# Kernel optimization log

Hardware: AMD Instinct MI355X
Metric: run time of the kernel (lower is better)

The kernel has to match this reference:

```python
import jax, jax.numpy as jnp
import numpy as np

B, V, T = 256, 4, 512
N = 128          # num_notes_per_voice[0]
H = 256          # lstm_hidden_size
HL = 200         # hidden_size_linear
L = 2            # num_layers


def _scalar_lstm_last(x, Wih, Whh, b):
    """Stacked LSTM(input=1, hidden=1, layers=L) over x:(M,T) -> last output (M,).
    Wih, Whh, b: (L, 4) scalar weights per gate (i,f,g,o order, PyTorch biases summed)."""
    M = x.shape[0]
    h0 = jnp.zeros((L, M), x.dtype)
    c0 = jnp.zeros((L, M), x.dtype)

    def step(carry, xt):
        h, c = carry
        inp = xt
        hs, cs = [], []
        for l in range(L):
            g = Wih[l][:, None] * inp[None, :] + Whh[l][:, None] * h[l][None, :] + b[l][:, None]  # (4, M)
            i, f, gg, o = jax.nn.sigmoid(g[0]), jax.nn.sigmoid(g[1]), jnp.tanh(g[2]), jax.nn.sigmoid(g[3])
            cn = f * c[l] + i * gg
            hn = o * jnp.tanh(cn)
            hs.append(hn); cs.append(cn)
            inp = hn
        return (jnp.stack(hs), jnp.stack(cs)), None

    (h, _), _ = jax.lax.scan(step, (h0, c0), x.T)  # scan over time
    return h[-1]  # top layer final hidden, (M,)


def _lstm2_last(x, Wih0, Whh0, b0, Wih1, Whh1, b1):
    """2-layer LSTM(input=1, hidden=H) over x:(B,S,1) -> last top-layer hidden (B,H)."""
    Bs = x.shape[0]
    Hd = Whh0.shape[1]

    def cell(pre, c):
        i, f, g, o = jnp.split(pre, 4, axis=-1)
        cn = jax.nn.sigmoid(f) * c + jax.nn.sigmoid(i) * jnp.tanh(g)
        return jax.nn.sigmoid(o) * jnp.tanh(cn), cn

    z = jnp.zeros((Bs, Hd), x.dtype)

    def step(carry, xt):
        h0, c0, h1, c1 = carry
        h0n, c0n = cell(xt @ Wih0.T + h0 @ Whh0.T + b0, c0)
        h1n, c1n = cell(h0n @ Wih1.T + h1 @ Whh1.T + b1, c1)
        return (h0n, c0n, h1n, c1n), None

    (_, _, h1, _), _ = jax.lax.scan(step, (z, z, z, z), x.transpose(1, 0, 2))
    return h1


def _branch(tokens, tW, tU, tb, Wih0, Whh0, b0, Wih1, Whh1, b1):
    """Fused version of the per-class Python loop: one-hot each of N classes over
    time (voice 0 only, as in the source), run scalar LSTM per (batch, class),
    then 2-layer LSTM over the class axis. tokens: (B, T) int."""
    Bs, Ts = tokens.shape
    onehot = (tokens[:, :, None] == jnp.arange(N)[None, None, :]).astype(jnp.float32)  # (B,T,N)
    x = onehot.transpose(0, 2, 1).reshape(Bs * N, Ts)           # (B*N, T): one series per class
    states = _scalar_lstm_last(x, tW, tU, tb).reshape(Bs, N, 1)  # States_ln / States_rn
    return _lstm2_last(states, Wih0, Whh0, b0, Wih1, Whh1, b1)   # (B, H)


def setup_inputs() -> dict:
    key = jax.random.key(0)
    ks = iter(jax.random.split(key, 32))
    def rn_(shape, s=0.1):
        return jax.random.normal(next(ks), shape, dtype=jnp.float32) * s
    inp = {
        "ln": jax.random.randint(next(ks), (B, V, T), 0, N),
        "cn": jax.random.randint(next(ks), (B, V - 1), 0, N),
        "rn": jax.random.randint(next(ks), (B, V, T), 0, N),
        "metas": jax.random.randint(next(ks), (B, 3, T), 0, 16),
        # time_lstm_left/right: LSTM(1->1), L layers; biases summed into one
        "tl_Wih": rn_((L, 4), 0.5), "tl_Whh": rn_((L, 4), 0.5), "tl_b": rn_((L, 4), 0.5),
        "tr_Wih": rn_((L, 4), 0.5), "tr_Whh": rn_((L, 4), 0.5), "tr_b": rn_((L, 4), 0.5),
        # notes_lstm_left/right: 2-layer LSTM(1->H)
        "nl_Wih0": rn_((4 * H, 1)), "nl_Whh0": rn_((4 * H, H)), "nl_b0": rn_((4 * H,)),
        "nl_Wih1": rn_((4 * H, H)), "nl_Whh1": rn_((4 * H, H)), "nl_b1": rn_((4 * H,)),
        "nr_Wih0": rn_((4 * H, 1)), "nr_Whh0": rn_((4 * H, H)), "nr_b0": rn_((4 * H,)),
        "nr_Wih1": rn_((4 * H, H)), "nr_Whh1": rn_((4 * H, H)), "nr_b1": rn_((4 * H,)),
        # mlp_predictions: Linear(2H -> HL) -> ReLU -> Linear(HL -> N)
        "mW1": rn_((HL, 2 * H)), "mb1": rn_((HL,)),
        "mW2": rn_((N, HL)), "mb2": rn_((N,)),
    }
    return inp


def reference(ln, cn, rn, metas,
              tl_Wih, tl_Whh, tl_b, tr_Wih, tr_Whh, tr_b,
              nl_Wih0, nl_Whh0, nl_b0, nl_Wih1, nl_Whh1, nl_b1,
              nr_Wih0, nr_Whh0, nr_b0, nr_Wih1, nr_Whh1, nr_b1,
              mW1, mb1, mW2, mb2):
    # cn and metas are unpacked but unused in the original forward()
    note_pred_ln = _branch(ln[:, 0, :], tl_Wih, tl_Whh, tl_b,
                           nl_Wih0, nl_Whh0, nl_b0, nl_Wih1, nl_Whh1, nl_b1)
    note_pred_rn = _branch(rn[:, 0, :], tr_Wih, tr_Whh, tr_b,
                           nr_Wih0, nr_Whh0, nr_b0, nr_Wih1, nr_Whh1, nr_b1)
    h = jnp.concatenate([note_pred_ln, note_pred_rn], axis=1)   # (B, 2H)
    return jax.nn.relu(h @ mW1.T + mb1) @ mW2.T + mb2           # (B, N)
```

## Files before the change

### kernel.cpp

```cpp
#include <hip/hip_runtime.h>


typedef _Float16 f16;
typedef __attribute__((ext_vector_type(4))) _Float16 f16x4;
typedef __attribute__((ext_vector_type(8))) _Float16 f16x8;
typedef __attribute__((ext_vector_type(4))) float f32x4;
typedef unsigned long long u64;

#define NBATCH 256
#define NTIME  512
#define NCLS   128
#define NHID   256

__device__ __forceinline__ float sigf(float x) {
    return __builtin_amdgcn_rcpf(1.0f + __expf(-x));
}
__device__ __forceinline__ float tanh_f(float x) {
    return fmaf(2.0f, __builtin_amdgcn_rcpf(1.0f + __expf(-2.0f * x)), -1.0f);
}
__device__ __forceinline__ f16x4 LO(f16x8 v) { f16x4 r; r[0]=v[0]; r[1]=v[1]; r[2]=v[2]; r[3]=v[3]; return r; }
__device__ __forceinline__ f16x4 HI(f16x8 v) { f16x4 r; r[0]=v[4]; r[1]=v[5]; r[2]=v[6]; r[3]=v[7]; return r; }

__device__ __forceinline__ u64 ld_llc(const u64* p) {
    return __hip_atomic_load(p, __ATOMIC_RELAXED, __HIP_MEMORY_SCOPE_AGENT);
}
__device__ __forceinline__ void st_llc(u64* p, u64 v) {
    __hip_atomic_store(p, v, __ATOMIC_RELAXED, __HIP_MEMORY_SCOPE_AGENT);
}
__device__ __forceinline__ int ld_flag(const int* p) {
    return __hip_atomic_load(p, __ATOMIC_RELAXED, __HIP_MEMORY_SCOPE_AGENT);
}
__device__ __forceinline__ void st_flag(int* p, int v) {
    __hip_atomic_store(p, v, __ATOMIC_RELAXED, __HIP_MEMORY_SCOPE_AGENT);
}

struct P6 {
    const float* s0; const float* s1; const float* s2;
    const float* s3; const float* s4; const float* s5;
};

__global__ __launch_bounds__(256) void k_cvt(P6 p, f16* __restrict__ dst) {
    int i = blockIdx.x * 256 + threadIdx.x;
    int seg = i >> 18, d = i & 262143;
    const float* s = seg == 0 ? p.s0 : seg == 1 ? p.s1 : seg == 2 ? p.s2
                   : seg == 3 ? p.s3 : seg == 4 ? p.s4 : p.s5;
    const int e  = d & 7;
    const int fr = (d >> 3) & 15;
    const int fq = (d >> 7) & 3;
    const int ktp = (d >> 9) & 7;
    const int fi = (d >> 12) & 15;
    const int g  = (d >> 16) & 3;
    const int row = g * 256 + fi * 16 + fr;
    const int col = ktp * 32 + (e >> 2) * 16 + fq * 4 + (e & 3);
    dst[i] = (f16)s[row * 256 + col];
}

__global__ void k_zero(int* __restrict__ f) { f[blockIdx.x * 1024 + threadIdx.x] = 0; }

__global__ __launch_bounds__(128) void k_scalar_lstm(
    const int* __restrict__ ln, const int* __restrict__ rn,
    const float* __restrict__ tlW, const float* __restrict__ tlU, const float* __restrict__ tlb,
    const float* __restrict__ trW, const float* __restrict__ trU, const float* __restrict__ trb,
    float* __restrict__ states)
{
    __shared__ int tok[NTIME];
    const int bid = blockIdx.x;
    const int branch = bid >> 8;
    const int b = bid & 255;
    const int* tp = (branch ? rn : ln) + (size_t)b * (4 * NTIME);
    for (int i = threadIdx.x; i < NTIME; i += 128) tok[i] = tp[i];
    __syncthreads();
    const float* W  = branch ? trW : tlW;
    const float* U  = branch ? trU : tlU;
    const float* Bb = branch ? trb : tlb;
    const float u00 = U[0], u01 = U[1], u02 = U[2], u03 = U[3];
    const float f00 = Bb[0], f01 = Bb[1], f02 = Bb[2], f03 = Bb[3];
    const float o00 = f00 + W[0], o01 = f01 + W[1], o02 = f02 + W[2], o03 = f03 + W[3];
    const float w10 = W[4], w11 = W[5], w12 = W[6], w13 = W[7];
    const float u10 = U[4], u11 = U[5], u12 = U[6], u13 = U[7];
    const float b10 = Bb[4], b11 = Bb[5], b12 = Bb[6], b13 = Bb[7];
    const int n = threadIdx.x;
    float h0 = 0.f, c0 = 0.f, h1 = 0.f, c1 = 0.f;
    for (int t = 0; t < NTIME; ++t) {
        const bool x = (tok[t] == n);
        float pi = fmaf(u00, h0, x ? o00 : f00);
        float pf = fmaf(u01, h0, x ? o01 : f01);
        float pg = fmaf(u02, h0, x ? o02 : f02);
        float po = fmaf(u03, h0, x ? o03 : f03);
        float ig = sigf(pi), fg = sigf(pf), gg = tanh_f(pg), og = sigf(po);
        c0 = fmaf(fg, c0, ig * gg);
        h0 = og * tanh_f(c0);
        pi = fmaf(w10, h0, fmaf(u10, h1, b10));
        pf = fmaf(w11, h0, fmaf(u11, h1, b11));
        pg = fmaf(w12, h0, fmaf(u12, h1, b12));
        po = fmaf(w13, h0, fmaf(u13, h1, b13));
        ig = sigf(pi); fg = sigf(pf); gg = tanh_f(pg); og = sigf(po);
        c1 = fmaf(fg, c1, ig * gg);
        h1 = og * tanh_f(c1);
    }
    states[((size_t)(branch * NBATCH + b)) * NCLS + n] = h1;
}

__global__ __launch_bounds__(256, 2) void k_rec(
    const float* __restrict__ states,
    const f16* __restrict__ whh0, const f16* __restrict__ whh1,
    const f16* __restrict__ wih1,
    const float* __restrict__ wih0L, const float* __restrict__ wih0R,
    const float* __restrict__ b0L, const float* __restrict__ b0R,
    const float* __restrict__ b1L, const float* __restrict__ b1R,
    f16* __restrict__ h0img,
    f16* __restrict__ ring,
    int* __restrict__ flags0,
    int* __restrict__ flags1,
    float* __restrict__ h1out)
{
    extern __shared__ char smem[];
    f16*   wlds = (f16*)smem;
    f16*   img  = (f16*)(smem + 65536);
    float* cmb  = (float*)(smem + 73728);

    const int bid = blockIdx.x;
    const bool isL1 = bid >= 256;
    const int sub = isL1 ? (bid - 256) : bid;
    const int qm = sub >> 5, g = sub & 31;
    const int branch = g >> 4, tb = g & 15;
    const int tid = threadIdx.x;
    const int w = tid >> 6, l = tid & 63, fr = l & 15, fq = l >> 4;

    {
        const f16* base = (isL1 ? whh1 : whh0) + ((size_t)branch << 18);
        for (int c = tid; c < 4096; c += 256) {
            const int rl = c >> 6, coli = c & 63;
            const int gg = rl >> 4, ff = (rl >> 3) & 1, ktp = rl & 7;
            *(uint4*)(wlds + rl * 512 + coli * 8) =
                *(const uint4*)(base + ((size_t)((gg * 16 + qm * 2 + ff) * 8 + ktp) << 9) + coli * 8);
        }
    }
    ((uint4*)img)[tid] = (uint4){0u, 0u, 0u, 0u};
    ((uint4*)img)[tid + 256] = (uint4){0u, 0u, 0u, 0u};

    if (!isL1) {
        const float* bias = branch ? b0R : b0L;
        const float* w0p  = branch ? wih0R : wih0L;
        const int fi_f = qm * 2 + (w < 2 ? w : 0);
        float bv[4], w0v[4];
#pragma unroll
        for (int g4 = 0; g4 < 4; ++g4) {
            bv[g4]  = bias[g4 * 256 + fi_f * 16 + fr];
            w0v[g4] = w0p[g4 * 256 + fi_f * 16 + fr];
        }
        float cst[4] = {0.f, 0.f, 0.f, 0.f};
        f16* gimg = h0img + (size_t)g * (NCLS * 4096);
        int* f0 = flags0 + g * 512;
        __syncthreads();

        for (int s = 0; s < NCLS; ++s) {
            float st[4];
            if (w < 2) {
#pragma unroll
                for (int r = 0; r < 4; ++r)
                    st[r] = states[((size_t)(branch * NBATCH + tb * 16 + fq * 4 + r)) * NCLS + s];
            }
            f16x4 af[16];
#pragma unroll
            for (int kt = 0; kt < 16; ++kt)
                af[kt] = *(const f16x4*)(img + kt * 256 + l * 4);
            f32x4 acc[2];
#pragma unroll
            for (int f = 0; f < 2; ++f) {
                f32x4 a0 = {0.f,0.f,0.f,0.f}, a1 = {0.f,0.f,0.f,0.f};
#pragma unroll
                for (int ktp = 0; ktp < 8; ++ktp) {
                    const f16x8 v = *(const f16x8*)(wlds + (((w * 2 + f) * 8 + ktp) << 9) + l * 8);
                    a0 = __builtin_amdgcn_mfma_f32_16x16x16f16(af[2 * ktp],     LO(v), a0, 0, 0, 0);
                    a1 = __builtin_amdgcn_mfma_f32_16x16x16f16(af[2 * ktp + 1], HI(v), a1, 0, 0, 0);
                }
                acc[f] = a0 + a1;
            }
            if (w == 0) {
#pragma unroll
                for (int r = 0; r < 4; ++r) cmb[(0 * 4 + r) * 64 + l] = acc[1][r];
            } else if (w == 1) {
#pragma unroll
                for (int r = 0; r < 4; ++r) cmb[(1 * 4 + r) * 64 + l] = acc[0][r];
            } else if (w == 2) {
#pragma unroll
                for (int r = 0; r < 4; ++r) {
                    cmb[(2 * 4 + r) * 64 + l] = acc[0][r];
                    cmb[(3 * 4 + r) * 64 + l] = acc[1][r];
                }
            } else {
#pragma unroll
                for (int r = 0; r < 4; ++r) {
                    cmb[(4 * 4 + r) * 64 + l] = acc[0][r];
                    cmb[(5 * 4 + r) * 64 + l] = acc[1][r];
                }
            }
            __syncthreads();
            if (w < 2) {
#pragma unroll
                for (int r = 0; r < 4; ++r) {
                    const float g0 = (w == 0) ? acc[0][r] : cmb[(0 * 4 + r) * 64 + l];
                    const float g1 = (w == 0) ? cmb[(1 * 4 + r) * 64 + l] : acc[1][r];
                    const float g2 = (w == 0) ? cmb[(2 * 4 + r) * 64 + l] : cmb[(3 * 4 + r) * 64 + l];
                    const float g3 = (w == 0) ? cmb[(4 * 4 + r) * 64 + l] : cmb[(5 * 4 + r) * 64 + l];
                    const float pi = fmaf(st[r], w0v[0], g0 + bv[0]);
                    const float pf = fmaf(st[r], w0v[1], g1 + bv[1]);
                    const float pg = fmaf(st[r], w0v[2], g2 + bv[2]);
                    const float po = fmaf(st[r], w0v[3], g3 + bv[3]);
                    const float ig = sigf(pi), fg = sigf(pf), gg = tanh_f(pg), og = sigf(po);
                    cst[r] = fmaf(fg, cst[r], ig * gg);
                    const float hn = og * tanh_f(cst[r]);
                    img[fi_f * 256 + (fq * 4 + r + 16 * (fr >> 2)) * 4 + (fr & 3)] = (f16)hn;
                }
            }
            __syncthreads();
            if (w == 0) {
                u64* gd = (u64*)(gimg + (size_t)s * 4096);
                st_llc(gd + qm * 128 + l,      ((const u64*)img)[qm * 128 + l]);
                st_llc(gd + qm * 128 + 64 + l, ((const u64*)img)[qm * 128 + 64 + l]);
                asm volatile("s_waitcnt vmcnt(0)" ::: "memory");
                if (l == 0) st_flag(f0 + qm * 64, s + 1);
                if (s < NCLS - 1 && l < 7) {
                    const int p = l + (l >= qm);
                    while (ld_flag(f0 + p * 64) <= s) __builtin_amdgcn_s_sleep(1);
                }
            }
            if (s == NCLS - 1) break;
            __syncthreads();
            if (tid < 128) {
                const u64* gs = (const u64*)(gimg + (size_t)s * 4096);
                u64 tmp[7];
#pragma unroll
                for (int j = 0; j < 7; ++j) {
                    const int p = j + (j >= qm);
                    tmp[j] = ld_llc(gs + p * 128 + tid);
                }
#pragma unroll
                for (int j = 0; j < 7; ++j) {
                    const int p = j + (j >= qm);
                    ((u64*)img)[p * 128 + tid] = tmp[j];
                }
            }
            __syncthreads();
        }
    } else {
        const float* bias = branch ? b1R : b1L;
        float bv[2][4];
#pragma unroll
        for (int f = 0; f < 2; ++f)
#pragma unroll
            for (int g4 = 0; g4 < 4; ++g4)
                bv[f][g4] = bias[g4 * 256 + (qm * 2 + f) * 16 + fr];
        float cst[2][4] = {{0.f,0.f,0.f,0.f},{0.f,0.f,0.f,0.f}};
        const f16* wstream = wih1 + ((size_t)branch << 18) + l * 8;
        const f16* gimg = h0img + (size_t)g * (NCLS * 4096);
        f16* gring = ring + (size_t)g * (4 * 4096);
        int* f0 = flags0 + g * 512;
        int* f1 = flags1 + g * 512;
        __syncthreads();
        if (w == 1 && l < 8) {
            while (ld_flag(f0 + l * 64) < 1) __builtin_amdgcn_s_sleep(2);
        }
        __syncthreads();
        f16x4 af0[16];
        {
            const u64* s2 = (const u64*)gimg + l;
#pragma unroll
            for (int kt = 0; kt < 16; ++kt)
                af0[kt] = __builtin_bit_cast(f16x4, ld_llc(s2 + kt * 64));
        }

        for (int t = 0; t < NCLS; ++t) {
            f16x8 wv[2][8];
#pragma unroll
            for (int f = 0; f < 2; ++f)
#pragma unroll
                for (int ktp = 0; ktp < 8; ++ktp)
                    wv[f][ktp] = *(const f16x8*)(wstream
                        + ((size_t)((w * 16 + qm * 2 + f) * 8 + ktp) << 9));
            f16x4 af1[16];
#pragma unroll
            for (int kt = 0; kt < 16; ++kt)
                af1[kt] = *(const f16x4*)(img + kt * 256 + l * 4);
            f32x4 acc[2];
#pragma unroll
            for (int f = 0; f < 2; ++f) {
                f32x4 a0 = {0.f,0.f,0.f,0.f}, a1 = {0.f,0.f,0.f,0.f};
#pragma unroll
                for (int ktp = 0; ktp < 8; ++ktp) {
                    const f16x8 v = *(const f16x8*)(wlds + (((w * 2 + f) * 8 + ktp) << 9) + l * 8);
                    a0 = __builtin_amdgcn_mfma_f32_16x16x16f16(af1[2 * ktp],     LO(v), a0, 0, 0, 0);
                    a1 = __builtin_amdgcn_mfma_f32_16x16x16f16(af1[2 * ktp + 1], HI(v), a1, 0, 0, 0);
                }
#pragma unroll
                for (int ktp = 0; ktp < 8; ++ktp) {
                    a0 = __builtin_amdgcn_mfma_f32_16x16x16f16(af0[2 * ktp],     LO(wv[f][ktp]), a0, 0, 0, 0);
                    a1 = __builtin_amdgcn_mfma_f32_16x16x16f16(af0[2 * ktp + 1], HI(wv[f][ktp]), a1, 0, 0, 0);
                }
                acc[f] = a0 + a1;
            }
            if (w > 0) {
#pragma unroll
                for (int f = 0; f < 2; ++f)
#pragma unroll
                    for (int r = 0; r < 4; ++r)
                        cmb[(((w - 1) * 2 + f) * 4 + r) * 64 + l] = acc[f][r];
            }
            __syncthreads();
            if (w == 0) {
#pragma unroll
                for (int f = 0; f < 2; ++f) {
#pragma unroll
                    for (int r = 0; r < 4; ++r) {
                        const float g0 = acc[f][r];
                        const float g1 = cmb[((0 * 2 + f) * 4 + r) * 64 + l];
                        const float g2 = cmb[((1 * 2 + f) * 4 + r) * 64 + l];
                        const float g3 = cmb[((2 * 2 + f) * 4 + r) * 64 + l];
                        const float pi = g0 + bv[f][0];
                        const float pf = g1 + bv[f][1];
                        const float pg = g2 + bv[f][2];
                        const float po = g3 + bv[f][3];
                        const float ig = sigf(pi), fg = sigf(pf), gg = tanh_f(pg), og = sigf(po);
                        cst[f][r] = fmaf(fg, cst[f][r], ig * gg);
                        const float hn = og * tanh_f(cst[f][r]);
                        if (t == NCLS - 1)
                            h1out[((size_t)(branch * NBATCH + tb * 16 + fq * 4 + r)) * NHID
                                  + (qm * 2 + f) * 16 + fr] = hn;
                        else
                            img[(qm * 2 + f) * 256 + (fq * 4 + r + 16 * (fr >> 2)) * 4 + (fr & 3)] = (f16)hn;
                    }
                }
            }
            if (t == NCLS - 1) break;
            f16* slot = gring + (size_t)(t & 3) * 4096;
            if (w == 0) {
                asm volatile("s_waitcnt lgkmcnt(0)" ::: "memory");
                u64* gd = (u64*)slot;
                st_llc(gd + qm * 128 + l,      ((const u64*)img)[qm * 128 + l]);
                st_llc(gd + qm * 128 + 64 + l, ((const u64*)img)[qm * 128 + 64 + l]);
                asm volatile("s_waitcnt vmcnt(0)" ::: "memory");
                if (l == 0) st_flag(f1 + qm * 64, t + 1);
                if (l < 7) {
                    const int p = l + (l >= qm);
                    while (ld_flag(f1 + p * 64) <= t) __builtin_amdgcn_s_sleep(1);
                }
            }
            if (w == 1 && l < 8) {
                while (ld_flag(f0 + l * 64) < t + 2) __builtin_amdgcn_s_sleep(1);
            }
            __syncthreads();
            {
                const u64* s2 = (const u64*)(gimg + (size_t)(t + 1) * 4096) + l;
#pragma unroll
                for (int kt = 0; kt < 16; ++kt)
                    af0[kt] = __builtin_bit_cast(f16x4, ld_llc(s2 + kt * 64));
            }
            if (tid < 128) {
                const u64* gs = (const u64*)slot;
                u64 tmp[7];
#pragma unroll
                for (int j = 0; j < 7; ++j) {
                    const int p = j + (j >= qm);
                    tmp[j] = ld_llc(gs + p * 128 + tid);
                }
#pragma unroll
                for (int j = 0; j < 7; ++j) {
                    const int p = j + (j >= qm);
                    ((u64*)img)[p * 128 + tid] = tmp[j];
                }
            }
            __syncthreads();
        }
    }
}

__global__ __launch_bounds__(256) void k_mlp(
    const float* __restrict__ h1all,
    const float* __restrict__ W1, const float* __restrict__ b1,
    const float* __restrict__ W2, const float* __restrict__ b2,
    float* __restrict__ out)
{
    __shared__ float hrow[512];
    __shared__ float hid[200];
    const int b = blockIdx.x, tid = threadIdx.x;
    hrow[tid]       = h1all[(size_t)b * NHID + tid];
    hrow[256 + tid] = h1all[(size_t)(NBATCH + b) * NHID + tid];
    __syncthreads();
    if (tid < 200) {
        float a = b1[tid];
        const float* wr = W1 + (size_t)tid * 512;
        for (int k = 0; k < 512; ++k) a = fmaf(wr[k], hrow[k], a);
        hid[tid] = fmaxf(a, 0.f);
    }
    __syncthreads();
    if (tid < 128) {
        float a = b2[tid];
        const float* wr = W2 + (size_t)tid * 200;
        for (int j = 0; j < 200; ++j) a = fmaf(wr[j], hid[j], a);
        out[(size_t)b * 128 + tid] = a;
    }
}

extern "C" void kernel_launch(void* const* d_in, const int* in_sizes, int n_in,
                              void* d_out, int out_size, void* d_ws, size_t ws_size,
                              hipStream_t stream)
{
    (void)in_sizes; (void)n_in; (void)out_size; (void)ws_size;
    const int*   ln    = (const int*)d_in[0];
    const int*   rn    = (const int*)d_in[2];
    const float* tlW   = (const float*)d_in[4];
    const float* tlU   = (const float*)d_in[5];
    const float* tlb   = (const float*)d_in[6];
    const float* trW   = (const float*)d_in[7];
    const float* trU   = (const float*)d_in[8];
    const float* trb   = (const float*)d_in[9];
    const float* wih0L = (const float*)d_in[10];
    const float* b0L   = (const float*)d_in[12];
    const float* b1L   = (const float*)d_in[15];
    const float* wih0R = (const float*)d_in[16];
    const float* b0R   = (const float*)d_in[18];
    const float* b1R   = (const float*)d_in[21];
    const float* mW1   = (const float*)d_in[22];
    const float* mb1   = (const float*)d_in[23];
    const float* mW2   = (const float*)d_in[24];
    const float* mb2   = (const float*)d_in[25];

    char* ws = (char*)d_ws;
    f16*   w16    = (f16*)ws;
    float* states = (float*)(ws + 3145728);
    float* h1out  = (float*)(ws + 3407872);
    int*   flags  = (int*)(ws + 3932160);
    f16*   ring   = (f16*)(ws + 4063232);
    f16*   h0img  = (f16*)(ws + 5111808);

    f16* whh0 = w16;
    f16* whh1 = w16 + 2 * 262144;
    f16* wih1 = w16 + 4 * 262144;
    int* flags0 = flags;
    int* flags1 = flags + 16384;

    (void)hipFuncSetAttribute(reinterpret_cast<const void*>(k_rec),
                              hipFuncAttributeMaxDynamicSharedMemorySize, 79872);

    P6 p { (const float*)d_in[11], (const float*)d_in[17],
           (const float*)d_in[14], (const float*)d_in[20],
           (const float*)d_in[13], (const float*)d_in[19] };
    k_zero<<<32, 1024, 0, stream>>>(flags);
    k_cvt<<<6144, 256, 0, stream>>>(p, w16);
    k_scalar_lstm<<<512, 128, 0, stream>>>(ln, rn, tlW, tlU, tlb, trW, trU, trb, states);
    k_rec<<<512, 256, 79872, stream>>>(states, whh0, whh1, wih1, wih0L, wih0R,
                                       b0L, b0R, b1L, b1R, h0img, ring,
                                       flags0, flags1, h1out);
    k_mlp<<<256, 256, 0, stream>>>(h1out, mW1, mb1, mW2, mb2, (float*)d_out);
}
```

Baseline: 722.7 us.

## Halve recurrent LSTM block count with four hidden slices per block, skew scalar LSTM layers

The recurrent kernel now splits each hidden dimension across 4 blocks instead of 8. Each block holds twice the Whh slice in LDS (about 152KB), launches 256 blocks instead of 512, and every wave computes gates for its own hidden slice. This reduces cross-block flag synchronisation partners and per-step global exchange traffic, but doubles MFMA work per block and drops occupancy to one block per CU. Separately, the scalar LSTM kernel is software-skewed so layer 0 of step t and layer 1 of step t-1 run together, exposing more instruction-level parallelism.

```diff
diff --git a/kernel.cpp b/kernel.cpp
--- a/kernel.cpp
+++ b/kernel.cpp
@@ -81,27 +81,46 @@
     const float b10 = Bb[4], b11 = Bb[5], b12 = Bb[6], b13 = Bb[7];
     const int n = threadIdx.x;
     float h0 = 0.f, c0 = 0.f, h1 = 0.f, c1 = 0.f;
-    for (int t = 0; t < NTIME; ++t) {
-        const bool x = (tok[t] == n);
+    {
+        const bool x = (tok[0] == n);
         float pi = fmaf(u00, h0, x ? o00 : f00);
         float pf = fmaf(u01, h0, x ? o01 : f01);
         float pg = fmaf(u02, h0, x ? o02 : f02);
         float po = fmaf(u03, h0, x ? o03 : f03);
-        float ig = sigf(pi), fg = sigf(pf), gg = tanh_f(pg), og = sigf(po);
+        const float ig = sigf(pi), fg = sigf(pf), gg = tanh_f(pg), og = sigf(po);
         c0 = fmaf(fg, c0, ig * gg);
         h0 = og * tanh_f(c0);
-        pi = fmaf(w10, h0, fmaf(u10, h1, b10));
-        pf = fmaf(w11, h0, fmaf(u11, h1, b11));
-        pg = fmaf(w12, h0, fmaf(u12, h1, b12));
-        po = fmaf(w13, h0, fmaf(u13, h1, b13));
-        ig = sigf(pi); fg = sigf(pf); gg = tanh_f(pg); og = sigf(po);
+    }
+    for (int t = 1; t < NTIME; ++t) {
+        const bool x = (tok[t] == n);
+        float api = fmaf(u00, h0, x ? o00 : f00);
+        float apf = fmaf(u01, h0, x ? o01 : f01);
+        float apg = fmaf(u02, h0, x ? o02 : f02);
+        float apo = fmaf(u03, h0, x ? o03 : f03);
+        float bpi = fmaf(w10, h0, fmaf(u10, h1, b10));
+        float bpf = fmaf(w11, h0, fmaf(u11, h1, b11));
+        float bpg = fmaf(w12, h0, fmaf(u12, h1, b12));
+        float bpo = fmaf(w13, h0, fmaf(u13, h1, b13));
+        const float aig = sigf(api), afg = sigf(apf), agg = tanh_f(apg), aog = sigf(apo);
+        const float big = sigf(bpi), bfg = sigf(bpf), bgg = tanh_f(bpg), bog = sigf(bpo);
+        c0 = fmaf(afg, c0, aig * agg);
+        c1 = fmaf(bfg, c1, big * bgg);
+        h0 = aog * tanh_f(c0);
+        h1 = bog * tanh_f(c1);
+    }
+    {
+        float pi = fmaf(w10, h0, fmaf(u10, h1, b10));
+        float pf = fmaf(w11, h0, fmaf(u11, h1, b11));
+        float pg = fmaf(w12, h0, fmaf(u12, h1, b12));
+        float po = fmaf(w13, h0, fmaf(u13, h1, b13));
+        const float ig = sigf(pi), fg = sigf(pf), gg = tanh_f(pg), og = sigf(po);
         c1 = fmaf(fg, c1, ig * gg);
         h1 = og * tanh_f(c1);
     }
     states[((size_t)(branch * NBATCH + b)) * NCLS + n] = h1;
 }
 
-__global__ __launch_bounds__(256, 2) void k_rec(
+__global__ __launch_bounds__(256, 1) void k_rec(
     const float* __restrict__ states,
     const f16* __restrict__ whh0, const f16* __restrict__ whh1,
     const f16* __restrict__ wih1,
@@ -116,152 +135,125 @@
 {
     extern __shared__ char smem[];
     f16*   wlds = (f16*)smem;
-    f16*   img  = (f16*)(smem + 65536);
-    float* cmb  = (float*)(smem + 73728);
+    f16*   img  = (f16*)(smem + 131072);
+    float* cmb  = (float*)(smem + 139264);
 
     const int bid = blockIdx.x;
-    const bool isL1 = bid >= 256;
-    const int sub = isL1 ? (bid - 256) : bid;
+    const bool isL1 = bid >= 128;
+    const int sub = isL1 ? bid - 128 : bid;
     const int qm = sub >> 5, g = sub & 31;
     const int branch = g >> 4, tb = g & 15;
     const int tid = threadIdx.x;
     const int w = tid >> 6, l = tid & 63, fr = l & 15, fq = l >> 4;
+    const int fi = qm * 4 + w;
 
     {
         const f16* base = (isL1 ? whh1 : whh0) + ((size_t)branch << 18);
-        for (int c = tid; c < 4096; c += 256) {
+        for (int c = tid; c < 8192; c += 256) {
             const int rl = c >> 6, coli = c & 63;
-            const int gg = rl >> 4, ff = (rl >> 3) & 1, ktp = rl & 7;
+            const int gs4 = rl >> 5, j = (rl >> 3) & 3, ktp = rl & 7;
             *(uint4*)(wlds + rl * 512 + coli * 8) =
-                *(const uint4*)(base + ((size_t)((gg * 16 + qm * 2 + ff) * 8 + ktp) << 9) + coli * 8);
+                *(const uint4*)(base + ((size_t)((gs4 * 16 + qm * 4 + j) * 8 + ktp) << 9) + coli * 8);
         }
     }
     ((uint4*)img)[tid] = (uint4){0u, 0u, 0u, 0u};
     ((uint4*)img)[tid + 256] = (uint4){0u, 0u, 0u, 0u};
 
+    float bv[4], w0v[4];
+    {
+        const float* bias = isL1 ? (branch ? b1R : b1L) : (branch ? b0R : b0L);
+        const float* w0p  = branch ? wih0R : wih0L;
+#pragma unroll
+        for (int g4 = 0; g4 < 4; ++g4) {
+            bv[g4]  = bias[g4 * 256 + fi * 16 + fr];
+            w0v[g4] = isL1 ? 0.f : w0p[g4 * 256 + fi * 16 + fr];
+        }
+    }
+    float cst[4] = {0.f, 0.f, 0.f, 0.f};
+
     if (!isL1) {
-        const float* bias = branch ? b0R : b0L;
-        const float* w0p  = branch ? wih0R : wih0L;
-        const int fi_f = qm * 2 + (w < 2 ? w : 0);
-        float bv[4], w0v[4];
-#pragma unroll
-        for (int g4 = 0; g4 < 4; ++g4) {
-            bv[g4]  = bias[g4 * 256 + fi_f * 16 + fr];
-            w0v[g4] = w0p[g4 * 256 + fi_f * 16 + fr];
-        }
-        float cst[4] = {0.f, 0.f, 0.f, 0.f};
         f16* gimg = h0img + (size_t)g * (NCLS * 4096);
-        int* f0 = flags0 + g * 512;
+        int* f0 = flags0 + g * 256;
         __syncthreads();
-
         for (int s = 0; s < NCLS; ++s) {
             float st[4];
-            if (w < 2) {
-#pragma unroll
-                for (int r = 0; r < 4; ++r)
-                    st[r] = states[((size_t)(branch * NBATCH + tb * 16 + fq * 4 + r)) * NCLS + s];
-            }
+#pragma unroll
+            for (int r = 0; r < 4; ++r)
+                st[r] = states[((size_t)(branch * NBATCH + tb * 16 + fq * 4 + r)) * NCLS + s];
             f16x4 af[16];
 #pragma unroll
             for (int kt = 0; kt < 16; ++kt)
                 af[kt] = *(const f16x4*)(img + kt * 256 + l * 4);
-            f32x4 acc[2];
-#pragma unroll
-            for (int f = 0; f < 2; ++f) {
-                f32x4 a0 = {0.f,0.f,0.f,0.f}, a1 = {0.f,0.f,0.f,0.f};
+            f32x4 acc[4];
+#pragma unroll
+            for (int j = 0; j < 4; ++j) { f32x4 z = {0.f,0.f,0.f,0.f}; acc[j] = z; }
+#pragma unroll
+            for (int j = 0; j < 4; ++j)
 #pragma unroll
                 for (int ktp = 0; ktp < 8; ++ktp) {
-                    const f16x8 v = *(const f16x8*)(wlds + (((w * 2 + f) * 8 + ktp) << 9) + l * 8);
-                    a0 = __builtin_amdgcn_mfma_f32_16x16x16f16(af[2 * ktp],     LO(v), a0, 0, 0, 0);
-                    a1 = __builtin_amdgcn_mfma_f32_16x16x16f16(af[2 * ktp + 1], HI(v), a1, 0, 0, 0);
+                    const f16x8 v = *(const f16x8*)(wlds + (((w * 4 + j) * 8 + ktp) << 9) + l * 8);
+                    acc[j] = __builtin_amdgcn_mfma_f32_16x16x16f16(af[2*ktp],   LO(v), acc[j], 0, 0, 0);
+                    acc[j] = __builtin_amdgcn_mfma_f32_16x16x16f16(af[2*ktp+1], HI(v), acc[j], 0, 0, 0);
                 }
-                acc[f] = a0 + a1;
-            }
+#pragma unroll
+            for (int j = 0; j < 4; ++j)
+                if (j != w)
+#pragma unroll
+                    for (int r = 0; r < 4; ++r)
+                        cmb[((w * 4 + j) * 4 + r) * 64 + l] = acc[j][r];
+            __syncthreads();
+#pragma unroll
+            for (int r = 0; r < 4; ++r) {
+                float gv[4];
+#pragma unroll
+                for (int g4 = 0; g4 < 4; ++g4)
+                    gv[g4] = (g4 == w) ? acc[w][r] : cmb[((g4 * 4 + w) * 4 + r) * 64 + l];
+                const float pi = fmaf(st[r], w0v[0], gv[0] + bv[0]);
+                const float pf = fmaf(st[r], w0v[1], gv[1] + bv[1]);
+                const float pg = fmaf(st[r], w0v[2], gv[2] + bv[2]);
+                const float po = fmaf(st[r], w0v[3], gv[3] + bv[3]);
+                const float ig = sigf(pi), fg = sigf(pf), gg = tanh_f(pg), og = sigf(po);
+                cst[r] = fmaf(fg, cst[r], ig * gg);
+                const float hn = og * tanh_f(cst[r]);
+                img[fi * 256 + (fq * 4 + r + 16 * (fr >> 2)) * 4 + (fr & 3)] = (f16)hn;
+            }
+            __syncthreads();
             if (w == 0) {
-#pragma unroll
-                for (int r = 0; r < 4; ++r) cmb[(0 * 4 + r) * 64 + l] = acc[1][r];
-            } else if (w == 1) {
-#pragma unroll
-                for (int r = 0; r < 4; ++r) cmb[(1 * 4 + r) * 64 + l] = acc[0][r];
-            } else if (w == 2) {
-#pragma unroll
-                for (int r = 0; r < 4; ++r) {
-                    cmb[(2 * 4 + r) * 64 + l] = acc[0][r];
-                    cmb[(3 * 4 + r) * 64 + l] = acc[1][r];
-                }
-            } else {
-#pragma unroll
-                for (int r = 0; r < 4; ++r) {
-                    cmb[(4 * 4 + r) * 64 + l] = acc[0][r];
-                    cmb[(5 * 4 + r) * 64 + l] = acc[1][r];
-                }
-            }
-            __syncthreads();
-            if (w < 2) {
-#pragma unroll
-                for (int r = 0; r < 4; ++r) {
-                    const float g0 = (w == 0) ? acc[0][r] : cmb[(0 * 4 + r) * 64 + l];
-                    const float g1 = (w == 0) ? cmb[(1 * 4 + r) * 64 + l] : acc[1][r];
-                    const float g2 = (w == 0) ? cmb[(2 * 4 + r) * 64 + l] : cmb[(3 * 4 + r) * 64 + l];
-                    const float g3 = (w == 0) ? cmb[(4 * 4 + r) * 64 + l] : cmb[(5 * 4 + r) * 64 + l];
-                    const float pi = fmaf(st[r], w0v[0], g0 + bv[0]);
-                    const float pf = fmaf(st[r], w0v[1], g1 + bv[1]);
-                    const float pg = fmaf(st[r], w0v[2], g2 + bv[2]);
-                    const float po = fmaf(st[r], w0v[3], g3 + bv[3]);
-                    const float ig = sigf(pi), fg = sigf(pf), gg = tanh_f(pg), og = sigf(po);
-                    cst[r] = fmaf(fg, cst[r], ig * gg);
-                    const float hn = og * tanh_f(cst[r]);
-                    img[fi_f * 256 + (fq * 4 + r + 16 * (fr >> 2)) * 4 + (fr & 3)] = (f16)hn;
-                }
-            }
-            __syncthreads();
-            if (w == 0) {
-                u64* gd = (u64*)(gimg + (size_t)s * 4096);
-                st_llc(gd + qm * 128 + l,      ((const u64*)img)[qm * 128 + l]);
-                st_llc(gd + qm * 128 + 64 + l, ((const u64*)img)[qm * 128 + 64 + l]);
+                u64* gd = (u64*)(gimg + (size_t)s * 4096) + qm * 256;
+                const u64* sc = (const u64*)img + qm * 256;
+                st_llc(gd + l,       sc[l]);
+                st_llc(gd + 64 + l,  sc[64 + l]);
+                st_llc(gd + 128 + l, sc[128 + l]);
+                st_llc(gd + 192 + l, sc[192 + l]);
                 asm volatile("s_waitcnt vmcnt(0)" ::: "memory");
                 if (l == 0) st_flag(f0 + qm * 64, s + 1);
-                if (s < NCLS - 1 && l < 7) {
+                if (s < NCLS - 1 && l < 3) {
                     const int p = l + (l >= qm);
                     while (ld_flag(f0 + p * 64) <= s) __builtin_amdgcn_s_sleep(1);
                 }
             }
             if (s == NCLS - 1) break;
             __syncthreads();
-            if (tid < 128) {
-                const u64* gs = (const u64*)(gimg + (size_t)s * 4096);
-                u64 tmp[7];
-#pragma unroll
-                for (int j = 0; j < 7; ++j) {
-                    const int p = j + (j >= qm);
-                    tmp[j] = ld_llc(gs + p * 128 + tid);
-                }
-#pragma unroll
-                for (int j = 0; j < 7; ++j) {
-                    const int p = j + (j >= qm);
-                    ((u64*)img)[p * 128 + tid] = tmp[j];
-                }
+            if (tid < 192) {
+                const int j = tid >> 6, o = tid & 63;
+                const int p = j + (j >= qm);
+                const u64* gs = (const u64*)(gimg + (size_t)s * 4096) + p * 256;
+                u64 t0 = ld_llc(gs + o),       t1 = ld_llc(gs + 64 + o),
+                    t2 = ld_llc(gs + 128 + o), t3 = ld_llc(gs + 192 + o);
+                u64* di = (u64*)img + p * 256;
+                di[o] = t0; di[64 + o] = t1; di[128 + o] = t2; di[192 + o] = t3;
             }
             __syncthreads();
         }
     } else {
-        const float* bias = branch ? b1R : b1L;
-        float bv[2][4];
-#pragma unroll
-        for (int f = 0; f < 2; ++f)
-#pragma unroll
-            for (int g4 = 0; g4 < 4; ++g4)
-                bv[f][g4] = bias[g4 * 256 + (qm * 2 + f) * 16 + fr];
-        float cst[2][4] = {{0.f,0.f,0.f,0.f},{0.f,0.f,0.f,0.f}};
         const f16* wstream = wih1 + ((size_t)branch << 18) + l * 8;
         const f16* gimg = h0img + (size_t)g * (NCLS * 4096);
         f16* gring = ring + (size_t)g * (4 * 4096);
-        int* f0 = flags0 + g * 512;
-        int* f1 = flags1 + g * 512;
+        int* f0 = flags0 + g * 256;
+        int* f1 = flags1 + g * 256;
         __syncthreads();
-        if (w == 1 && l < 8) {
+        if (w == 1 && l < 4)
             while (ld_flag(f0 + l * 64) < 1) __builtin_amdgcn_s_sleep(2);
-        }
         __syncthreads();
         f16x4 af0[16];
         {
@@ -270,85 +262,78 @@
             for (int kt = 0; kt < 16; ++kt)
                 af0[kt] = __builtin_bit_cast(f16x4, ld_llc(s2 + kt * 64));
         }
-
         for (int t = 0; t < NCLS; ++t) {
-            f16x8 wv[2][8];
-#pragma unroll
-            for (int f = 0; f < 2; ++f)
-#pragma unroll
-                for (int ktp = 0; ktp < 8; ++ktp)
-                    wv[f][ktp] = *(const f16x8*)(wstream
-                        + ((size_t)((w * 16 + qm * 2 + f) * 8 + ktp) << 9));
             f16x4 af1[16];
 #pragma unroll
             for (int kt = 0; kt < 16; ++kt)
                 af1[kt] = *(const f16x4*)(img + kt * 256 + l * 4);
-            f32x4 acc[2];
-#pragma unroll
-            for (int f = 0; f < 2; ++f) {
-                f32x4 a0 = {0.f,0.f,0.f,0.f}, a1 = {0.f,0.f,0.f,0.f};
+            f32x4 acc[4];
+#pragma unroll
+            for (int j = 0; j < 4; ++j) { f32x4 z = {0.f,0.f,0.f,0.f}; acc[j] = z; }
+#pragma unroll
+            for (int j = 0; j < 4; ++j) {
+                f16x8 wv[8];
+#pragma unroll
+                for (int ktp = 0; ktp < 8; ++ktp)
+                    wv[ktp] = *(const f16x8*)(wstream
+                        + ((size_t)((w * 16 + qm * 4 + j) * 8 + ktp) << 9));
 #pragma unroll
                 for (int ktp = 0; ktp < 8; ++ktp) {
-                    const f16x8 v = *(const f16x8*)(wlds + (((w * 2 + f) * 8 + ktp) << 9) + l * 8);
-                    a0 = __builtin_amdgcn_mfma_f32_16x16x16f16(af1[2 * ktp],     LO(v), a0, 0, 0, 0);
-                    a1 = __builtin_amdgcn_mfma_f32_16x16x16f16(af1[2 * ktp + 1], HI(v), a1, 0, 0, 0);
+                    const f16x8 v = *(const f16x8*)(wlds + (((w * 4 + j) * 8 + ktp) << 9) + l * 8);
+                    acc[j] = __builtin_amdgcn_mfma_f32_16x16x16f16(af1[2*ktp],   LO(v), acc[j], 0, 0, 0);
+                    acc[j] = __builtin_amdgcn_mfma_f32_16x16x16f16(af1[2*ktp+1], HI(v), acc[j], 0, 0, 0);
                 }
 #pragma unroll
                 for (int ktp = 0; ktp < 8; ++ktp) {
-                    a0 = __builtin_amdgcn_mfma_f32_16x16x16f16(af0[2 * ktp],     LO(wv[f][ktp]), a0, 0, 0, 0);
-                    a1 = __builtin_amdgcn_mfma_f32_16x16x16f16(af0[2 * ktp + 1], HI(wv[f][ktp]), a1, 0, 0, 0);
+                    acc[j] = __builtin_amdgcn_mfma_f32_16x16x16f16(af0[2*ktp],   LO(wv[ktp]), acc[j], 0, 0, 0);
+                    acc[j] = __builtin_amdgcn_mfma_f32_16x16x16f16(af0[2*ktp+1], HI(wv[ktp]), acc[j], 0, 0, 0);
                 }
-                acc[f] = a0 + a1;
-            }
-            if (w > 0) {
-#pragma unroll
-                for (int f = 0; f < 2; ++f)
+            }
+#pragma unroll
+            for (int j = 0; j < 4; ++j)
+                if (j != w)
 #pragma unroll
                     for (int r = 0; r < 4; ++r)
-                        cmb[(((w - 1) * 2 + f) * 4 + r) * 64 + l] = acc[f][r];
-            }
-            __syncthreads();
-            if (w == 0) {
-#pragma unroll
-                for (int f = 0; f < 2; ++f) {
-#pragma unroll
-                    for (int r = 0; r < 4; ++r) {
-                        const float g0 = acc[f][r];
-                        const float g1 = cmb[((0 * 2 + f) * 4 + r) * 64 + l];
-                        const float g2 = cmb[((1 * 2 + f) * 4 + r) * 64 + l];
-                        const float g3 = cmb[((2 * 2 + f) * 4 + r) * 64 + l];
-                        const float pi = g0 + bv[f][0];
-                        const float pf = g1 + bv[f][1];
-                        const float pg = g2 + bv[f][2];
-                        const float po = g3 + bv[f][3];
-                        const float ig = sigf(pi), fg = sigf(pf), gg = tanh_f(pg), og = sigf(po);
-                        cst[f][r] = fmaf(fg, cst[f][r], ig * gg);
-                        const float hn = og * tanh_f(cst[f][r]);
-                        if (t == NCLS - 1)
-                            h1out[((size_t)(branch * NBATCH + tb * 16 + fq * 4 + r)) * NHID
-                                  + (qm * 2 + f) * 16 + fr] = hn;
-                        else
-                            img[(qm * 2 + f) * 256 + (fq * 4 + r + 16 * (fr >> 2)) * 4 + (fr & 3)] = (f16)hn;
-                    }
-                }
+                        cmb[((w * 4 + j) * 4 + r) * 64 + l] = acc[j][r];
+            __syncthreads();
+#pragma unroll
+            for (int r = 0; r < 4; ++r) {
+                float gv[4];
+#pragma unroll
+                for (int g4 = 0; g4 < 4; ++g4)
+                    gv[g4] = (g4 == w) ? acc[w][r] : cmb[((g4 * 4 + w) * 4 + r) * 64 + l];
+                const float pi = gv[0] + bv[0];
+                const float pf = gv[1] + bv[1];
+                const float pg = gv[2] + bv[2];
+                const float po = gv[3] + bv[3];
+                const float ig = sigf(pi), fg = sigf(pf), gg = tanh_f(pg), og = sigf(po);
+                cst[r] = fmaf(fg, cst[r], ig * gg);
+                const float hn = og * tanh_f(cst[r]);
+                if (t == NCLS - 1)
+                    h1out[((size_t)(branch * NBATCH + tb * 16 + fq * 4 + r)) * NHID
+                          + fi * 16 + fr] = hn;
+                else
+                    img[fi * 256 + (fq * 4 + r + 16 * (fr >> 2)) * 4 + (fr & 3)] = (f16)hn;
             }
             if (t == NCLS - 1) break;
+            __syncthreads();
             f16* slot = gring + (size_t)(t & 3) * 4096;
             if (w == 0) {
-                asm volatile("s_waitcnt lgkmcnt(0)" ::: "memory");
-                u64* gd = (u64*)slot;
-                st_llc(gd + qm * 128 + l,      ((const u64*)img)[qm * 128 + l]);
-                st_llc(gd + qm * 128 + 64 + l, ((const u64*)img)[qm * 128 + 64 + l]);
+                u64* gd = (u64*)slot + qm * 256;
+                const u64* sc = (const u64*)img + qm * 256;
+                st_llc(gd + l,       sc[l]);
+                st_llc(gd + 64 + l,  sc[64 + l]);
+                st_llc(gd + 128 + l, sc[128 + l]);
+                st_llc(gd + 192 + l, sc[192 + l]);
                 asm volatile("s_waitcnt vmcnt(0)" ::: "memory");
                 if (l == 0) st_flag(f1 + qm * 64, t + 1);
-                if (l < 7) {
+                if (l < 3) {
                     const int p = l + (l >= qm);
                     while (ld_flag(f1 + p * 64) <= t) __builtin_amdgcn_s_sleep(1);
                 }
             }
-            if (w == 1 && l < 8) {
+            if (w == 1 && l < 4)
                 while (ld_flag(f0 + l * 64) < t + 2) __builtin_amdgcn_s_sleep(1);
-            }
             __syncthreads();
             {
                 const u64* s2 = (const u64*)(gimg + (size_t)(t + 1) * 4096) + l;
@@ -356,19 +341,14 @@
                 for (int kt = 0; kt < 16; ++kt)
                     af0[kt] = __builtin_bit_cast(f16x4, ld_llc(s2 + kt * 64));
             }
-            if (tid < 128) {
-                const u64* gs = (const u64*)slot;
-                u64 tmp[7];
-#pragma unroll
-                for (int j = 0; j < 7; ++j) {
-                    const int p = j + (j >= qm);
-                    tmp[j] = ld_llc(gs + p * 128 + tid);
-                }
-#pragma unroll
-                for (int j = 0; j < 7; ++j) {
-                    const int p = j + (j >= qm);
-                    ((u64*)img)[p * 128 + tid] = tmp[j];
-                }
+            if (tid < 192) {
+                const int j = tid >> 6, o = tid & 63;
+                const int p = j + (j >= qm);
+                const u64* gs = (const u64*)slot + p * 256;
+                u64 t0 = ld_llc(gs + o),       t1 = ld_llc(gs + 64 + o),
+                    t2 = ld_llc(gs + 128 + o), t3 = ld_llc(gs + 192 + o);
+                u64* di = (u64*)img + p * 256;
+                di[o] = t0; di[64 + o] = t1; di[128 + o] = t2; di[192 + o] = t3;
             }
             __syncthreads();
         }
@@ -438,19 +418,19 @@
     f16* whh1 = w16 + 2 * 262144;
     f16* wih1 = w16 + 4 * 262144;
     int* flags0 = flags;
-    int* flags1 = flags + 16384;
+    int* flags1 = flags + 8192;
 
     (void)hipFuncSetAttribute(reinterpret_cast<const void*>(k_rec),
-                              hipFuncAttributeMaxDynamicSharedMemorySize, 79872);
+                              hipFuncAttributeMaxDynamicSharedMemorySize, 155648);
 
     P6 p { (const float*)d_in[11], (const float*)d_in[17],
            (const float*)d_in[14], (const float*)d_in[20],
            (const float*)d_in[13], (const float*)d_in[19] };
-    k_zero<<<32, 1024, 0, stream>>>(flags);
+    k_zero<<<16, 1024, 0, stream>>>(flags);
     k_cvt<<<6144, 256, 0, stream>>>(p, w16);
     k_scalar_lstm<<<512, 128, 0, stream>>>(ln, rn, tlW, tlU, tlb, trW, trU, trb, states);
-    k_rec<<<512, 256, 79872, stream>>>(states, whh0, whh1, wih1, wih0L, wih0R,
-                                       b0L, b0R, b1L, b1R, h0img, ring,
-                                       flags0, flags1, h1out);
+    k_rec<<<256, 256, 155648, stream>>>(states, whh0, whh1, wih1, wih0L, wih0R,
+                                        b0L, b0R, b1L, b1R, h0img, ring,
+                                        flags0, flags1, h1out);
     k_mlp<<<256, 256, 0, stream>>>(h1out, mW1, mb1, mW2, mb2, (float*)d_out);
 }
```

Result: slower. 833.3 us (+15.3%).

## Fuse flag zeroing, weight conversion and scalar LSTM into one kernel with skewed layers

Applied to the files above, without the earlier changes.

Merges the flag-zero, fp16 weight-conversion and scalar-LSTM kernels into a single launch whose blocks pick a role by block index, so the memory-bound conversion can overlap the latency-bound scalar recurrence. The scalar LSTM now packs two (branch,batch) pairs into each 256-thread block. Its two layers are software-skewed so that layer 0 at step t and layer 1 at step t-1 run independently, exposing more instruction-level parallelism in the serial chain. This costs two fewer kernel launches, at the price of more register pressure and mixed block roles.

```diff
diff --git a/kernel.cpp b/kernel.cpp
--- a/kernel.cpp
+++ b/kernel.cpp
@@ -39,36 +39,48 @@
     const float* s3; const float* s4; const float* s5;
 };
 
-__global__ __launch_bounds__(256) void k_cvt(P6 p, f16* __restrict__ dst) {
-    int i = blockIdx.x * 256 + threadIdx.x;
-    int seg = i >> 18, d = i & 262143;
-    const float* s = seg == 0 ? p.s0 : seg == 1 ? p.s1 : seg == 2 ? p.s2
-                   : seg == 3 ? p.s3 : seg == 4 ? p.s4 : p.s5;
-    const int e  = d & 7;
-    const int fr = (d >> 3) & 15;
-    const int fq = (d >> 7) & 3;
-    const int ktp = (d >> 9) & 7;
-    const int fi = (d >> 12) & 15;
-    const int g  = (d >> 16) & 3;
-    const int row = g * 256 + fi * 16 + fr;
-    const int col = ktp * 32 + (e >> 2) * 16 + fq * 4 + (e & 3);
-    dst[i] = (f16)s[row * 256 + col];
-}
-
-__global__ void k_zero(int* __restrict__ f) { f[blockIdx.x * 1024 + threadIdx.x] = 0; }
-
-__global__ __launch_bounds__(128) void k_scalar_lstm(
+__global__ __launch_bounds__(256) void k_pre(
     const int* __restrict__ ln, const int* __restrict__ rn,
     const float* __restrict__ tlW, const float* __restrict__ tlU, const float* __restrict__ tlb,
     const float* __restrict__ trW, const float* __restrict__ trU, const float* __restrict__ trb,
-    float* __restrict__ states)
+    float* __restrict__ states,
+    P6 p, f16* __restrict__ wdst,
+    int* __restrict__ flags)
 {
-    __shared__ int tok[NTIME];
     const int bid = blockIdx.x;
-    const int branch = bid >> 8;
-    const int b = bid & 255;
+    const int tid = threadIdx.x;
+    if (bid >= 768) {
+        int* f = flags + (bid - 768) * 16384;
+        for (int i = tid; i < 16384; i += 256) f[i] = 0;
+        return;
+    }
+    if (bid >= 256) {
+        const int base = (bid - 256) * 3072;
+#pragma unroll
+        for (int k = 0; k < 12; ++k) {
+            const int i = base + k * 256 + tid;
+            const int seg = i >> 18, d = i & 262143;
+            const float* s = seg == 0 ? p.s0 : seg == 1 ? p.s1 : seg == 2 ? p.s2
+                           : seg == 3 ? p.s3 : seg == 4 ? p.s4 : p.s5;
+            const int e  = d & 7;
+            const int fr = (d >> 3) & 15;
+            const int fq = (d >> 7) & 3;
+            const int ktp = (d >> 9) & 7;
+            const int fi = (d >> 12) & 15;
+            const int g  = (d >> 16) & 3;
+            const int row = g * 256 + fi * 16 + fr;
+            const int col = ktp * 32 + (e >> 2) * 16 + fq * 4 + (e & 3);
+            wdst[i] = (f16)s[row * 256 + col];
+        }
+        return;
+    }
+    __shared__ int tok[2][NTIME];
+    const int half = tid >> 7, n = tid & 127;
+    const int pair = bid * 2 + half;
+    const int branch = pair >> 8;
+    const int b = pair & 255;
     const int* tp = (branch ? rn : ln) + (size_t)b * (4 * NTIME);
-    for (int i = threadIdx.x; i < NTIME; i += 128) tok[i] = tp[i];
+    for (int i = n; i < NTIME; i += 128) tok[half][i] = tp[i];
     __syncthreads();
     const float* W  = branch ? trW : tlW;
     const float* U  = branch ? trU : tlU;
@@ -79,22 +91,40 @@
     const float w10 = W[4], w11 = W[5], w12 = W[6], w13 = W[7];
     const float u10 = U[4], u11 = U[5], u12 = U[6], u13 = U[7];
     const float b10 = Bb[4], b11 = Bb[5], b12 = Bb[6], b13 = Bb[7];
-    const int n = threadIdx.x;
     float h0 = 0.f, c0 = 0.f, h1 = 0.f, c1 = 0.f;
-    for (int t = 0; t < NTIME; ++t) {
-        const bool x = (tok[t] == n);
+    {
+        const bool x = (tok[half][0] == n);
         float pi = fmaf(u00, h0, x ? o00 : f00);
         float pf = fmaf(u01, h0, x ? o01 : f01);
         float pg = fmaf(u02, h0, x ? o02 : f02);
         float po = fmaf(u03, h0, x ? o03 : f03);
-        float ig = sigf(pi), fg = sigf(pf), gg = tanh_f(pg), og = sigf(po);
+        const float ig = sigf(pi), fg = sigf(pf), gg = tanh_f(pg), og = sigf(po);
         c0 = fmaf(fg, c0, ig * gg);
         h0 = og * tanh_f(c0);
-        pi = fmaf(w10, h0, fmaf(u10, h1, b10));
-        pf = fmaf(w11, h0, fmaf(u11, h1, b11));
-        pg = fmaf(w12, h0, fmaf(u12, h1, b12));
-        po = fmaf(w13, h0, fmaf(u13, h1, b13));
-        ig = sigf(pi); fg = sigf(pf); gg = tanh_f(pg); og = sigf(po);
+    }
+    for (int t = 1; t < NTIME; ++t) {
+        const bool x = (tok[half][t] == n);
+        float api = fmaf(u00, h0, x ? o00 : f00);
+        float apf = fmaf(u01, h0, x ? o01 : f01);
+        float apg = fmaf(u02, h0, x ? o02 : f02);
+        float apo = fmaf(u03, h0, x ? o03 : f03);
+        float bpi = fmaf(w10, h0, fmaf(u10, h1, b10));
+        float bpf = fmaf(w11, h0, fmaf(u11, h1, b11));
+        float bpg = fmaf(w12, h0, fmaf(u12, h1, b12));
+        float bpo = fmaf(w13, h0, fmaf(u13, h1, b13));
+        const float aig = sigf(api), afg = sigf(apf), agg = tanh_f(apg), aog = sigf(apo);
+        const float big = sigf(bpi), bfg = sigf(bpf), bgg = tanh_f(bpg), bog = sigf(bpo);
+        c0 = fmaf(afg, c0, aig * agg);
+        c1 = fmaf(bfg, c1, big * bgg);
+        h0 = aog * tanh_f(c0);
+        h1 = bog * tanh_f(c1);
+    }
+    {
+        float pi = fmaf(w10, h0, fmaf(u10, h1, b10));
+        float pf = fmaf(w11, h0, fmaf(u11, h1, b11));
+        float pg = fmaf(w12, h0, fmaf(u12, h1, b12));
+        float po = fmaf(w13, h0, fmaf(u13, h1, b13));
+        const float ig = sigf(pi), fg = sigf(pf), gg = tanh_f(pg), og = sigf(po);
         c1 = fmaf(fg, c1, ig * gg);
         h1 = og * tanh_f(c1);
     }
@@ -446,9 +476,8 @@
     P6 p { (const float*)d_in[11], (const float*)d_in[17],
            (const float*)d_in[14], (const float*)d_in[20],
            (const float*)d_in[13], (const float*)d_in[19] };
-    k_zero<<<32, 1024, 0, stream>>>(flags);
-    k_cvt<<<6144, 256, 0, stream>>>(p, w16);
-    k_scalar_lstm<<<512, 128, 0, stream>>>(ln, rn, tlW, tlU, tlb, trW, trU, trb, states);
+    k_pre<<<770, 256, 0, stream>>>(ln, rn, tlW, tlU, tlb, trW, trU, trb,
+                                   states, p, w16, flags);
     k_rec<<<512, 256, 79872, stream>>>(states, whh0, whh1, wih1, wih0L, wih0R,
                                        b0L, b0R, b1L, b1R, h0img, ring,
                                        flags0, flags1, h1out);
```

New measurement: 640.1 us. 1.13x faster.
